# Performance work log

Hardware: AMD Instinct MI355X
Metric: run time of the kernel (lower is better)

Reference implementation:

```python
import jax, jax.numpy as jnp
import numpy as np

BN_EPS = 1e-5
CLAMP = 1e-10


def _three_nn(q, p):
    # q: (B,N,3) query points, p: (B,M,3) reference points
    # returns dist (B,N,3) euclidean distance to 3 nearest, idx (B,N,3)
    d2 = (jnp.sum(q * q, -1)[:, :, None] + jnp.sum(p * p, -1)[:, None, :]
          - 2.0 * jnp.einsum('bnd,bmd->bnm', q, p))  # (B,N,M)
    neg_vals, idx = jax.lax.top_k(-d2, 3)
    dist = jnp.sqrt(jnp.maximum(-neg_vals, 1e-20))
    return dist, idx


def _gather(feats_t, idx):
    # feats_t: (B,M,C), idx: (B,N,3) -> (B,N,3,C)
    return jax.vmap(lambda f, i: f[i])(feats_t, idx)


def _conv_bn_relu(x, W, b, g, beta):
    # x: (B,Cin,N); 1x1 Conv1d + BatchNorm1d (training-mode batch stats) + relu
    y = jnp.einsum('oc,bcn->bon', W, x) + b[None, :, None]
    mean = jnp.mean(y, axis=(0, 2), keepdims=True)
    var = jnp.mean((y - mean) ** 2, axis=(0, 2), keepdims=True)
    y = (y - mean) * jax.lax.rsqrt(var + BN_EPS)
    y = y * g[None, :, None] + beta[None, :, None]
    return jax.nn.relu(y)


def setup_inputs() -> dict:
    key = jax.random.key(0)
    ks = jax.random.split(key, 10)
    B, N, M, C2, C1 = 4, 8192, 2048, 256, 128
    inp = {
        'xyz1': jax.random.normal(ks[0], (B, 3, N), jnp.float32),
        'xyz2': jax.random.normal(ks[1], (B, 3, M), jnp.float32),
        'norm1': jax.random.normal(ks[2], (B, 3, N), jnp.float32),
        'norm2': jax.random.normal(ks[3], (B, 3, M), jnp.float32),
        'points1': jax.random.normal(ks[4], (B, C1, N), jnp.float32),
        'points2': jax.random.normal(ks[5], (B, C2, M), jnp.float32),
        'W0': jax.random.normal(ks[6], (256, C2 + C1), jnp.float32) * 0.05,
        'b0': jax.random.normal(ks[7], (256,), jnp.float32) * 0.05,
        'g0': jnp.ones((256,), jnp.float32),
        'be0': jnp.zeros((256,), jnp.float32),
        'W1': jax.random.normal(ks[8], (128, 256), jnp.float32) * 0.05,
        'b1': jax.random.normal(ks[9], (128,), jnp.float32) * 0.05,
        'g1': jnp.ones((128,), jnp.float32),
        'be1': jnp.zeros((128,), jnp.float32),
    }
    return inp


def reference(xyz1, xyz2, norm1, norm2, points1, points2,
              W0, b0, g0, be0, W1, b1, g1, be1):
    B, _, N = xyz1.shape
    # 3-NN search
    dist, idx = _three_nn(jnp.transpose(xyz1, (0, 2, 1)),
                          jnp.transpose(xyz2, (0, 2, 1)))  # (B,N,3)
    # normal distance between query normals and gathered neighbor normals
    grouped_norm = _gather(jnp.transpose(norm2, (0, 2, 1)), idx)        # (B,N,3,3)
    diff = jnp.transpose(norm1, (0, 2, 1))[:, :, None, :] - grouped_norm
    norm_dist = jnp.sqrt(jnp.sum(diff * diff, -1))                       # (B,N,3)
    # distance weights
    recip_dist = 1.0 / jnp.maximum(dist, CLAMP)
    weight = recip_dist / jnp.sum(recip_dist, 2, keepdims=True)
    # normal weights
    recip_nd = 1.0 / jnp.maximum(norm_dist, CLAMP)
    norm_weight = recip_nd / jnp.sum(recip_nd, 2, keepdims=True)
    weight = weight * norm_weight                                        # (B,N,3)
    # three_interpolate: weighted gather of points2
    gathered_pts = _gather(jnp.transpose(points2, (0, 2, 1)), idx)       # (B,N,3,C)
    interpolated = jnp.einsum('bnkc,bnk->bcn', gathered_pts, weight)     # (B,C,N)
    new_points = jnp.concatenate([interpolated, points1], axis=1)        # (B,C+C1,N)
    new_points = _conv_bn_relu(new_points, W0, b0, g0, be0)
    new_points = _conv_bn_relu(new_points, W1, b1, g1, be1)
    return new_points
```

## Files before the change

kernel.cpp:

```cpp
#include <hip/hip_runtime.h>
#include <hip/hip_bf16.h>
#include <cstdint>
#include <cstddef>

static constexpr int BB   = 4;
static constexpr int NN   = 8192;
static constexpr int MM   = 2048;
static constexpr int C1   = 128;
static constexpr int C2   = 256;
static constexpr int CH0  = C2 + C1;
static constexpr int O0   = 256;
static constexpr int O1   = 128;
static constexpr int NCOL = BB * NN;
static constexpr float BN_EPS = 1e-5f;

static constexpr int REC0 = 64;
static constexpr int REC1 = 32;

using u16 = unsigned short;
typedef __attribute__((ext_vector_type(8))) short short8;
typedef __attribute__((ext_vector_type(4))) float f32x4;

static __device__ __forceinline__ float bf2f(u16 u) {
    union { unsigned int i; float f; } v; v.i = ((unsigned int)u) << 16; return v.f;
}
static __device__ __forceinline__ u16 f2bf(float f) {
    union { float f; unsigned int i; } v; v.f = f;
    unsigned int r = (v.i + 0x7fffu + ((v.i >> 16) & 1u)) >> 16;
    return (u16)r;
}

__global__ __launch_bounds__(256) void fused_pre_kernel(
        const float* __restrict__ xyz1,  const float* __restrict__ xyz2,
        const float* __restrict__ norm1, const float* __restrict__ norm2,
        int* __restrict__ idxOut, float* __restrict__ wOut,
        const float* __restrict__ points2, u16* __restrict__ p2T,
        const float* __restrict__ points1, u16* __restrict__ p1T,
        const float* __restrict__ W0f, u16* __restrict__ W0b,
        const float* __restrict__ W1f, u16* __restrict__ W1b,
        float* __restrict__ part0, float* __restrict__ part1) {
#pragma clang fp contract(off)
    __shared__ union { float4 pts[1024]; float tile[32][33]; } sm;
    int id = blockIdx.x;
    int t  = threadIdx.x;

    if (id >= 7680) {
        int flat = (id - 7680) * 256 + t;
        if (flat < REC0 * 512) part0[flat] = 0.f;
        else part1[flat - REC0 * 512] = 0.f;
        return;
    }
    if (id >= 1024) {
        int pid = id - 1024;
        if (pid < 6144) {
            const float* in; u16* out; int R, C, b, c0, r0;
            if (pid < 2048) {
                in = points2; out = p2T; R = C2; C = MM;
                b = pid >> 9; int rem = pid & 511;
                c0 = (rem & 63) * 32; r0 = (rem >> 6) * 32;
            } else {
                int id2 = pid - 2048;
                in = points1; out = p1T; R = C1; C = NN;
                b = id2 >> 10; int rem = id2 & 1023;
                c0 = (rem & 255) * 32; r0 = (rem >> 8) * 32;
            }
            int tx = t & 31, ty = t >> 5;
            const float* pin = in + (size_t)b * R * C;
            u16* pout = out + (size_t)b * R * C;
#pragma unroll
            for (int j = 0; j < 4; ++j) {
                int r = ty + j * 8;
                sm.tile[r][tx] = pin[(size_t)(r0 + r) * C + (c0 + tx)];
            }
            __syncthreads();
#pragma unroll
            for (int j = 0; j < 4; ++j) {
                int c = ty + j * 8;
                pout[(size_t)(c0 + c) * R + (r0 + tx)] = f2bf(sm.tile[tx][c]);
            }
        } else {
            int i = (pid - 6144) * 256 + t;
            if (i < O0 * CH0) W0b[i] = f2bf(W0f[i]);
            else {
                int i2 = i - O0 * CH0;
                if (i2 < O1 * O0) W1b[i2] = f2bf(W1f[i2]);
            }
        }
        return;
    }

    int b    = id >> 8;
    int nblk = id & 255;
    int j    = t & 7;

    int n = nblk * 32 + (t >> 3);
    const float* x1 = xyz1 + (size_t)b * 3 * NN;
    float qx = x1[n], qy = x1[NN + n], qz = x1[2 * NN + n];
    float qq = __builtin_fmaf(qx, qx, __builtin_fmaf(qy, qy, qz * qz));

    const float* x2 = xyz2 + (size_t)b * 3 * MM;

    float d0 = 3.4e38f, d1 = 3.4e38f, d2v = 3.4e38f;
    int   i0 = 0, i1 = 0, i2 = 0;

    for (int chunk = 0; chunk < MM / 1024; ++chunk) {
        __syncthreads();
        for (int i = t; i < 1024; i += 256) {
            int m = chunk * 1024 + i;
            float px = x2[m];
            float py = x2[MM + m];
            float pz = x2[2 * MM + m];
            float pp = __builtin_fmaf(px, px, __builtin_fmaf(py, py, pz * pz));
            sm.pts[i] = make_float4(-2.0f * px, -2.0f * py, -2.0f * pz, pp);
        }
        __syncthreads();

#pragma unroll 8
        for (int s = 0; s < 1024 / 8; ++s) {
            int ml = s * 8 + j;
            float4 P = sm.pts[ml];
            float d  = __builtin_fmaf(qx, P.x,
                        __builtin_fmaf(qy, P.y,
                         __builtin_fmaf(qz, P.z, qq + P.w)));
            if (d < d2v) {
                int m = chunk * 1024 + ml;
                if (d < d1) {
                    if (d < d0) { d2v = d1; i2 = i1; d1 = d0; i1 = i0; d0 = d; i0 = m; }
                    else        { d2v = d1; i2 = i1; d1 = d;  i1 = m; }
                } else          { d2v = d;  i2 = m; }
            }
        }
    }

#pragma unroll
    for (int k = 1; k <= 4; k <<= 1) {
        float e0 = __shfl_xor(d0, k, 64), e1 = __shfl_xor(d1, k, 64), e2 = __shfl_xor(d2v, k, 64);
        int   f0 = __shfl_xor(i0, k, 64), f1 = __shfl_xor(i1, k, 64), f2 = __shfl_xor(i2, k, 64);
        float ed[3] = {e0, e1, e2}; int ef[3] = {f0, f1, f2};
#pragma unroll
        for (int e = 0; e < 3; ++e) {
            float dd = ed[e]; int ff = ef[e];
            bool b2 = (dd < d2v) || (dd == d2v && ff < i2);
            if (b2) {
                bool b1 = (dd < d1) || (dd == d1 && ff < i1);
                if (b1) {
                    d2v = d1; i2 = i1;
                    bool b0 = (dd < d0) || (dd == d0 && ff < i0);
                    if (b0) { d1 = d0; i1 = i0; d0 = dd; i0 = ff; }
                    else    { d1 = dd; i1 = ff; }
                } else { d2v = dd; i2 = ff; }
            }
        }
    }

    if (j == 0) {
        float s0 = sqrtf(fmaxf(d0, 1e-20f));
        float s1 = sqrtf(fmaxf(d1, 1e-20f));
        float s2 = sqrtf(fmaxf(d2v, 1e-20f));
        float r0 = 1.0f / fmaxf(s0, 1e-10f);
        float r1 = 1.0f / fmaxf(s1, 1e-10f);
        float r2 = 1.0f / fmaxf(s2, 1e-10f);
        float rs = (r0 + r1) + r2;
        float w0 = r0 / rs, w1 = r1 / rs, w2 = r2 / rs;

        const float* nm1 = norm1 + (size_t)b * 3 * NN;
        const float* nm2 = norm2 + (size_t)b * 3 * MM;
        float ax = nm1[n], ay = nm1[NN + n], az = nm1[2 * NN + n];
        float nd[3]; int ii[3] = {i0, i1, i2};
#pragma unroll
        for (int k = 0; k < 3; ++k) {
            int ik = ii[k];
            float dx = ax - nm2[ik];
            float dy = ay - nm2[MM + ik];
            float dz = az - nm2[2 * MM + ik];
            nd[k] = sqrtf((dx * dx + dy * dy) + dz * dz);
        }
        float m0 = 1.0f / fmaxf(nd[0], 1e-10f);
        float m1 = 1.0f / fmaxf(nd[1], 1e-10f);
        float m2 = 1.0f / fmaxf(nd[2], 1e-10f);
        float ms = (m0 + m1) + m2;

        int col = b * NN + n;
        idxOut[col * 3 + 0] = i0;
        idxOut[col * 3 + 1] = i1;
        idxOut[col * 3 + 2] = i2;
        wOut[col * 3 + 0] = w0 * (m0 / ms);
        wOut[col * 3 + 1] = w1 * (m1 / ms);
        wOut[col * 3 + 2] = w2 * (m2 / ms);
    }
}

__global__ __launch_bounds__(256, 2) void gemm0_kernel(
        const u16* __restrict__ A,
        const u16* __restrict__ Bt,
        const u16* __restrict__ p1T,
        const int* __restrict__ idx,
        const float* __restrict__ w,
        u16* __restrict__ Ct,
        const float* __restrict__ bias,
        float* __restrict__ partials) {
    constexpr int KDIM = CH0;
    constexpr int COLT = 64;
    constexpr int KT  = KDIM / 64;
    constexpr int NI  = COLT / 32;
    constexpr int ASZ = 256 * 64;
    constexpr int BSZ = COLT * 64;
    __shared__ u16 smem[2 * ASZ + 2 * BSZ];

    int t   = threadIdx.x;
    int l   = t & 63;
    int wv  = t >> 6;
    int rl  = l >> 3;
    int cg_ = ((l & 7) ^ rl) * 8;
    int cb0 = blockIdx.x * COLT;
    int lm  = l & 15;
    int q   = l >> 4;
    int wm0 = (wv & 1) * 64;
    int wn0 = (wv >> 1) * (COLT / 2);

    int colg = cb0 + (t >> 2);
    int vi0 = idx[colg * 3 + 0], vi1 = idx[colg * 3 + 1], vi2 = idx[colg * 3 + 2];
    float vw0 = w[colg * 3 + 0], vw1 = w[colg * 3 + 1], vw2 = w[colg * 3 + 2];
    const u16* p2base = Bt + (size_t)(cb0 >> 13) * MM * C2;

    auto stage = [&](int buf, int k0) {
#pragma unroll
        for (int iss = 0; iss < 8; ++iss) {
            int row = wv * 64 + iss * 8;
            const u16* g = A + (size_t)(row + rl) * KDIM + k0 + cg_;
            __builtin_amdgcn_global_load_lds(
                (const __attribute__((address_space(1))) unsigned int*)g,
                (__attribute__((address_space(3))) unsigned int*)(&smem[buf * ASZ + row * 64]),
                16, 0, 0);
        }
        if (k0 < C2) {
            int row = t >> 2;
            int kc  = (t & 3) * 16;
            const u16* bp = p2base + k0 + kc;
            const u16* r0p = bp + (size_t)vi0 * C2;
            const u16* r1p = bp + (size_t)vi1 * C2;
            const u16* r2p = bp + (size_t)vi2 * C2;
            union { uint4 v; u16 u[8]; } x0, x1, x2, y0, y1, y2, lo, hi;
            x0.v = *(const uint4*)r0p; y0.v = *(const uint4*)(r0p + 8);
            x1.v = *(const uint4*)r1p; y1.v = *(const uint4*)(r1p + 8);
            x2.v = *(const uint4*)r2p; y2.v = *(const uint4*)(r2p + 8);
#pragma unroll
            for (int e = 0; e < 8; ++e) {
                lo.u[e] = f2bf(vw0 * bf2f(x0.u[e]) + vw1 * bf2f(x1.u[e]) + vw2 * bf2f(x2.u[e]));
                hi.u[e] = f2bf(vw0 * bf2f(y0.u[e]) + vw1 * bf2f(y1.u[e]) + vw2 * bf2f(y2.u[e]));
            }
            int c0 = kc >> 3;
            u16* dstB = &smem[2 * ASZ + buf * BSZ + row * 64];
            *(uint4*)&dstB[((c0)     ^ (row & 7)) * 8] = lo.v;
            *(uint4*)&dstB[((c0 + 1) ^ (row & 7)) * 8] = hi.v;
        } else {
#pragma unroll
            for (int iss = 0; iss < 2; ++iss) {
                int row = wv * 16 + iss * 8;
                const u16* g = p1T + (size_t)(cb0 + row + rl) * C1 + (k0 - C2) + cg_;
                __builtin_amdgcn_global_load_lds(
                    (const __attribute__((address_space(1))) unsigned int*)g,
                    (__attribute__((address_space(3))) unsigned int*)(&smem[2 * ASZ + buf * BSZ + row * 64]),
                    16, 0, 0);
            }
        }
    };

    f32x4 acc[8][NI] = {};

    stage(0, 0);
    for (int kt = 0; kt < KT; ++kt) {
        __syncthreads();
        if (kt + 1 < KT) stage((kt + 1) & 1, (kt + 1) * 64);
        const u16* As = &smem[(kt & 1) * ASZ];
        const u16* Bs = &smem[2 * ASZ + (kt & 1) * BSZ];
#pragma unroll
        for (int ks = 0; ks < 2; ++ks) {
            int csw = ((ks * 4 + q) ^ (lm & 7)) * 8;
            short8 av[8], bv[NI];
#pragma unroll
            for (int mi = 0; mi < 8; ++mi) {
                int mrow = (mi >> 2) * 128 + wm0 + (mi & 3) * 16;
                av[mi] = *(const short8*)&As[(mrow + lm) * 64 + csw];
            }
#pragma unroll
            for (int ni = 0; ni < NI; ++ni)
                bv[ni] = *(const short8*)&Bs[(wn0 + ni * 16 + lm) * 64 + csw];
#pragma unroll
            for (int mi = 0; mi < 8; ++mi)
#pragma unroll
                for (int ni = 0; ni < NI; ++ni)
                    acc[mi][ni] = __builtin_amdgcn_mfma_f32_16x16x32_bf16(
                        av[mi], bv[ni], acc[mi][ni], 0, 0, 0);
        }
    }

    u16*   Cs   = smem;
    float* reds = (float*)&smem[COLT * 264];

    __syncthreads();
    reds[t] = 0.f; reds[256 + t] = 0.f;
    __syncthreads();

#pragma unroll
    for (int mi = 0; mi < 8; ++mi) {
        int chL = (mi >> 2) * 128 + wm0 + (mi & 3) * 16 + q * 4;
        float bv4[4];
#pragma unroll
        for (int r = 0; r < 4; ++r) bv4[r] = bias[chL + r];
        float s[4]  = {0.f, 0.f, 0.f, 0.f};
        float s2[4] = {0.f, 0.f, 0.f, 0.f};
#pragma unroll
        for (int ni = 0; ni < NI; ++ni) {
            int colL = wn0 + ni * 16 + lm;
            union { u16 u[4]; uint2 d; } pk;
#pragma unroll
            for (int r = 0; r < 4; ++r) {
                float v = acc[mi][ni][r] + bv4[r];
                s[r]  += v;
                s2[r] += v * v;
                pk.u[r] = f2bf(v);
            }
            *(uint2*)&Cs[colL * 264 + chL] = pk.d;
        }
#pragma unroll
        for (int r = 0; r < 4; ++r) {
            float a = s[r], b2 = s2[r];
#pragma unroll
            for (int off = 1; off < 16; off <<= 1) {
                a  += __shfl_xor(a, off, 64);
                b2 += __shfl_xor(b2, off, 64);
            }
            if (lm == 0) {
                atomicAdd(&reds[chL + r], a);
                atomicAdd(&reds[256 + chL + r], b2);
            }
        }
    }
    __syncthreads();

    {
        int c = t >> 2, h = t & 3;
        const u16* src = &Cs[c * 264 + h * 64];
        u16* dst = Ct + (size_t)(cb0 + c) * O0 + h * 64;
#pragma unroll
        for (int jj = 0; jj < 8; ++jj)
            *(uint4*)(dst + jj * 8) = *(const uint4*)(src + jj * 8);
    }
    int recIdx = blockIdx.x & (REC0 - 1);
    atomicAdd(&partials[(size_t)recIdx * 512 + t], reds[t]);
    atomicAdd(&partials[(size_t)recIdx * 512 + 256 + t], reds[256 + t]);
}

__global__ __launch_bounds__(256) void gemm1_kernel(const u16* __restrict__ A,
                                                    const u16* __restrict__ Bt,
                                                    u16* __restrict__ Ct,
                                                    const float* __restrict__ bias,
                                                    const float* __restrict__ redB,
                                                    const float* __restrict__ gB,
                                                    const float* __restrict__ beB,
                                                    float invN,
                                                    float* __restrict__ partials) {
    constexpr int KDIM = O0;
    constexpr int COLT = 64;
    constexpr int KT  = KDIM / 64;
    constexpr int NI  = COLT / 32;
    constexpr int ASZ = 128 * 64;
    constexpr int BSZ = COLT * 64;
    __shared__ u16 smem[2 * ASZ + 2 * BSZ];
    __shared__ float sSc[KDIM];
    __shared__ float sSh[KDIM];

    int t   = threadIdx.x;
    int l   = t & 63;
    int wv  = t >> 6;
    int rl  = l >> 3;
    int cg_ = ((l & 7) ^ rl) * 8;
    int cb0 = blockIdx.x * COLT;
    int lm  = l & 15;
    int q   = l >> 4;
    int wm0 = (wv & 1) * 64;
    int wn0 = (wv >> 1) * (COLT / 2);

    {
        float s = 0.f, s2 = 0.f;
#pragma unroll 8
        for (int i = 0; i < REC0; ++i) {
            s  += redB[i * 512 + t];
            s2 += redB[i * 512 + 256 + t];
        }
        float mean = s * invN;
        float var  = fmaxf(s2 * invN - mean * mean, 0.f);
        float inv  = rsqrtf(var + BN_EPS);
        float sc   = gB[t] * inv;
        sSc[t] = sc;
        sSh[t] = beB[t] - mean * sc;
        __syncthreads();
    }

    auto stage = [&](int buf, int k0) {
#pragma unroll
        for (int iss = 0; iss < 4; ++iss) {
            int row = wv * 32 + iss * 8;
            const u16* g = A + (size_t)(row + rl) * KDIM + k0 + cg_;
            __builtin_amdgcn_global_load_lds(
                (const __attribute__((address_space(1))) unsigned int*)g,
                (__attribute__((address_space(3))) unsigned int*)(&smem[buf * ASZ + row * 64]),
                16, 0, 0);
        }
        {
            int row = t >> 2;
            int kc  = (t & 3) * 16;
            const u16* gp = Bt + (size_t)(cb0 + row) * KDIM + k0 + kc;
            union { uint4 v; u16 u[8]; } lo, hi;
            lo.v = *(const uint4*)gp;
            hi.v = *(const uint4*)(gp + 8);
#pragma unroll
            for (int e = 0; e < 8; ++e) {
                float f0 = bf2f(lo.u[e]);
                lo.u[e] = f2bf(fmaxf(f0 * sSc[k0 + kc + e] + sSh[k0 + kc + e], 0.f));
                float f1 = bf2f(hi.u[e]);
                hi.u[e] = f2bf(fmaxf(f1 * sSc[k0 + kc + 8 + e] + sSh[k0 + kc + 8 + e], 0.f));
            }
            int c0 = kc >> 3;
            u16* dstB = &smem[2 * ASZ + buf * BSZ + row * 64];
            *(uint4*)&dstB[((c0)     ^ (row & 7)) * 8] = lo.v;
            *(uint4*)&dstB[((c0 + 1) ^ (row & 7)) * 8] = hi.v;
        }
    };

    f32x4 acc[4][NI] = {};

    stage(0, 0);
    for (int kt = 0; kt < KT; ++kt) {
        __syncthreads();
        if (kt + 1 < KT) stage((kt + 1) & 1, (kt + 1) * 64);
        const u16* As = &smem[(kt & 1) * ASZ];
        const u16* Bs = &smem[2 * ASZ + (kt & 1) * BSZ];
#pragma unroll
        for (int ks = 0; ks < 2; ++ks) {
            int csw = ((ks * 4 + q) ^ (lm & 7)) * 8;
            short8 av[4], bv[NI];
#pragma unroll
            for (int mi = 0; mi < 4; ++mi)
                av[mi] = *(const short8*)&As[(wm0 + mi * 16 + lm) * 64 + csw];
#pragma unroll
            for (int ni = 0; ni < NI; ++ni)
                bv[ni] = *(const short8*)&Bs[(wn0 + ni * 16 + lm) * 64 + csw];
#pragma unroll
            for (int mi = 0; mi < 4; ++mi)
#pragma unroll
                for (int ni = 0; ni < NI; ++ni)
                    acc[mi][ni] = __builtin_amdgcn_mfma_f32_16x16x32_bf16(
                        av[mi], bv[ni], acc[mi][ni], 0, 0, 0);
        }
    }

    u16*   Cs   = smem;
    float* reds = (float*)&smem[COLT * 136];

    __syncthreads();
    if (t < 256) reds[t] = 0.f;
    __syncthreads();

#pragma unroll
    for (int mi = 0; mi < 4; ++mi) {
        int chL = wm0 + mi * 16 + q * 4;
        float bv4[4];
#pragma unroll
        for (int r = 0; r < 4; ++r) bv4[r] = bias[chL + r];
        float s[4]  = {0.f, 0.f, 0.f, 0.f};
        float s2[4] = {0.f, 0.f, 0.f, 0.f};
#pragma unroll
        for (int ni = 0; ni < NI; ++ni) {
            int colL = wn0 + ni * 16 + lm;
            union { u16 u[4]; uint2 d; } pk;
#pragma unroll
            for (int r = 0; r < 4; ++r) {
                float v = acc[mi][ni][r] + bv4[r];
                s[r]  += v;
                s2[r] += v * v;
                pk.u[r] = f2bf(v);
            }
            *(uint2*)&Cs[colL * 136 + chL] = pk.d;
        }
#pragma unroll
        for (int r = 0; r < 4; ++r) {
            float a = s[r], b2 = s2[r];
#pragma unroll
            for (int off = 1; off < 16; off <<= 1) {
                a  += __shfl_xor(a, off, 64);
                b2 += __shfl_xor(b2, off, 64);
            }
            if (lm == 0) {
                atomicAdd(&reds[chL + r], a);
                atomicAdd(&reds[128 + chL + r], b2);
            }
        }
    }
    __syncthreads();

    for (int u = t; u < COLT * 2; u += 256) {
        int c = u >> 1, h = u & 1;
        const u16* src = &Cs[c * 136 + h * 64];
        u16* dst = Ct + (size_t)(cb0 + c) * O1 + h * 64;
#pragma unroll
        for (int jj = 0; jj < 8; ++jj)
            *(uint4*)(dst + jj * 8) = *(const uint4*)(src + jj * 8);
    }
    int recIdx = blockIdx.x & (REC1 - 1);
    atomicAdd(&partials[(size_t)recIdx * 256 + t], reds[t]);
}

__global__ __launch_bounds__(256) void finalize_kernel(const u16* __restrict__ y1T,
                                                       const float* __restrict__ part1,
                                                       const float* __restrict__ g1,
                                                       const float* __restrict__ be1,
                                                       float invN,
                                                       float* __restrict__ out) {
    __shared__ float tile[64][129];
    __shared__ float sc[O1], sh[O1];
    int t  = threadIdx.x;
    int b  = blockIdx.y;
    int n0 = blockIdx.x * 64;

    if (t < O1) {
        float s = 0.f, s2 = 0.f;
#pragma unroll 8
        for (int i = 0; i < REC1; ++i) {
            s  += part1[i * 256 + t];
            s2 += part1[i * 256 + 128 + t];
        }
        float mean = s * invN;
        float var  = fmaxf(s2 * invN - mean * mean, 0.f);
        float inv  = rsqrtf(var + BN_EPS);
        float scv  = g1[t] * inv;
        sc[t] = scv;
        sh[t] = be1[t] - mean * scv;
    }
    __syncthreads();

#pragma unroll
    for (int it = 0; it < 32; ++it) {
        int flat = it * 256 + t;
        int cl = flat >> 7;
        int c  = flat & 127;
        int col = b * NN + n0 + cl;
        float v = bf2f(y1T[(size_t)col * O1 + c]);
        tile[cl][c] = fmaxf(v * sc[c] + sh[c], 0.f);
    }
    __syncthreads();
#pragma unroll
    for (int it = 0; it < 32; ++it) {
        int flat = it * 256 + t;
        int c  = flat >> 6;
        int nl = flat & 63;
        out[(size_t)b * O1 * NN + (size_t)c * NN + n0 + nl] = tile[nl][c];
    }
}

extern "C" void kernel_launch(void* const* d_in, const int* in_sizes, int n_in,
                              void* d_out, int out_size, void* d_ws, size_t ws_size,
                              hipStream_t stream) {
    (void)in_sizes; (void)n_in; (void)out_size; (void)ws_size;

    const float* xyz1    = (const float*)d_in[0];
    const float* xyz2    = (const float*)d_in[1];
    const float* norm1   = (const float*)d_in[2];
    const float* norm2   = (const float*)d_in[3];
    const float* points1 = (const float*)d_in[4];
    const float* points2 = (const float*)d_in[5];
    const float* W0f     = (const float*)d_in[6];
    const float* b0      = (const float*)d_in[7];
    const float* g0      = (const float*)d_in[8];
    const float* be0     = (const float*)d_in[9];
    const float* W1f     = (const float*)d_in[10];
    const float* b1      = (const float*)d_in[11];
    const float* g1      = (const float*)d_in[12];
    const float* be1     = (const float*)d_in[13];
    float* out = (float*)d_out;

    char* w8 = (char*)d_ws;
    size_t off = 0;
    auto carve = [&](size_t bytes) { void* p = w8 + off; off += (bytes + 255) & ~(size_t)255; return p; };
    int*   idxW   = (int*)  carve((size_t)NCOL * 3 * sizeof(int));
    float* wW     = (float*)carve((size_t)NCOL * 3 * sizeof(float));
    u16*   p2T    = (u16*)  carve((size_t)BB * MM * C2 * 2);
    u16*   p1T    = (u16*)  carve((size_t)BB * NN * C1 * 2);
    u16*   W0b    = (u16*)  carve((size_t)O0 * CH0 * 2);
    u16*   W1b    = (u16*)  carve((size_t)O1 * O0 * 2);
    u16*   y0T    = (u16*)  carve((size_t)NCOL * O0 * 2);
    u16*   y1T    = (u16*)  carve((size_t)NCOL * O1 * 2);
    float* part0  = (float*)carve((size_t)REC0 * 512 * sizeof(float));
    float* part1  = (float*)carve((size_t)REC1 * 256 * sizeof(float));

    const float invN = 1.0f / (float)NCOL;

    fused_pre_kernel<<<7840, 256, 0, stream>>>(
        xyz1, xyz2, norm1, norm2, idxW, wW,
        points2, p2T, points1, p1T, W0f, W0b, W1f, W1b, part0, part1);

    gemm0_kernel<<<NCOL / 64, 256, 0, stream>>>(
        W0b, p2T, p1T, idxW, wW, y0T, b0, part0);

    gemm1_kernel<<<NCOL / 64, 256, 0, stream>>>(
        W1b, y0T, y1T, b1, part0, g0, be0, invN, part1);

    finalize_kernel<<<dim3(NN / 64, BB), 256, 0, stream>>>(y1T, part1, g1, be1, invN, out);
}
```

Measured before the change: 180.8 us.

## Split three-point interpolation out of GEMM0 into a separate kernel

```diff
diff --git a/kernel.cpp b/kernel.cpp
--- a/kernel.cpp
+++ b/kernel.cpp
@@ -190,12 +190,41 @@
     }
 }
 
+__global__ __launch_bounds__(256) void interp_kernel(
+        const u16* __restrict__ p2T,
+        const int* __restrict__ idx,
+        const float* __restrict__ w,
+        u16* __restrict__ xI) {
+    int t   = threadIdx.x;
+    int col = blockIdx.x * 32 + (t >> 3);
+    int kc  = (t & 7) * 32;
+
+    int vi0 = idx[col * 3 + 0], vi1 = idx[col * 3 + 1], vi2 = idx[col * 3 + 2];
+    float vw0 = w[col * 3 + 0], vw1 = w[col * 3 + 1], vw2 = w[col * 3 + 2];
+
+    const u16* bp  = p2T + (size_t)(col >> 13) * MM * C2 + kc;
+    const u16* r0p = bp + (size_t)vi0 * C2;
+    const u16* r1p = bp + (size_t)vi1 * C2;
+    const u16* r2p = bp + (size_t)vi2 * C2;
+    u16* dst = xI + (size_t)col * C2 + kc;
+
+#pragma unroll
+    for (int jj = 0; jj < 4; ++jj) {
+        union { uint4 v; u16 u[8]; } x0, x1, x2, o;
+        x0.v = *(const uint4*)(r0p + jj * 8);
+        x1.v = *(const uint4*)(r1p + jj * 8);
+        x2.v = *(const uint4*)(r2p + jj * 8);
+#pragma unroll
+        for (int e = 0; e < 8; ++e)
+            o.u[e] = f2bf(vw0 * bf2f(x0.u[e]) + vw1 * bf2f(x1.u[e]) + vw2 * bf2f(x2.u[e]));
+        *(uint4*)(dst + jj * 8) = o.v;
+    }
+}
+
 __global__ __launch_bounds__(256, 2) void gemm0_kernel(
         const u16* __restrict__ A,
-        const u16* __restrict__ Bt,
+        const u16* __restrict__ xI,
         const u16* __restrict__ p1T,
-        const int* __restrict__ idx,
-        const float* __restrict__ w,
         u16* __restrict__ Ct,
         const float* __restrict__ bias,
         float* __restrict__ partials) {
@@ -218,11 +247,6 @@
     int wm0 = (wv & 1) * 64;
     int wn0 = (wv >> 1) * (COLT / 2);
 
-    int colg = cb0 + (t >> 2);
-    int vi0 = idx[colg * 3 + 0], vi1 = idx[colg * 3 + 1], vi2 = idx[colg * 3 + 2];
-    float vw0 = w[colg * 3 + 0], vw1 = w[colg * 3 + 1], vw2 = w[colg * 3 + 2];
-    const u16* p2base = Bt + (size_t)(cb0 >> 13) * MM * C2;
-
     auto stage = [&](int buf, int k0) {
 #pragma unroll
         for (int iss = 0; iss < 8; ++iss) {
@@ -233,36 +257,16 @@
                 (__attribute__((address_space(3))) unsigned int*)(&smem[buf * ASZ + row * 64]),
                 16, 0, 0);
         }
-        if (k0 < C2) {
-            int row = t >> 2;
-            int kc  = (t & 3) * 16;
-            const u16* bp = p2base + k0 + kc;
-            const u16* r0p = bp + (size_t)vi0 * C2;
-            const u16* r1p = bp + (size_t)vi1 * C2;
-            const u16* r2p = bp + (size_t)vi2 * C2;
-            union { uint4 v; u16 u[8]; } x0, x1, x2, y0, y1, y2, lo, hi;
-            x0.v = *(const uint4*)r0p; y0.v = *(const uint4*)(r0p + 8);
-            x1.v = *(const uint4*)r1p; y1.v = *(const uint4*)(r1p + 8);
-            x2.v = *(const uint4*)r2p; y2.v = *(const uint4*)(r2p + 8);
-#pragma unroll
-            for (int e = 0; e < 8; ++e) {
-                lo.u[e] = f2bf(vw0 * bf2f(x0.u[e]) + vw1 * bf2f(x1.u[e]) + vw2 * bf2f(x2.u[e]));
-                hi.u[e] = f2bf(vw0 * bf2f(y0.u[e]) + vw1 * bf2f(y1.u[e]) + vw2 * bf2f(y2.u[e]));
-            }
-            int c0 = kc >> 3;
-            u16* dstB = &smem[2 * ASZ + buf * BSZ + row * 64];
-            *(uint4*)&dstB[((c0)     ^ (row & 7)) * 8] = lo.v;
-            *(uint4*)&dstB[((c0 + 1) ^ (row & 7)) * 8] = hi.v;
-        } else {
-#pragma unroll
-            for (int iss = 0; iss < 2; ++iss) {
-                int row = wv * 16 + iss * 8;
-                const u16* g = p1T + (size_t)(cb0 + row + rl) * C1 + (k0 - C2) + cg_;
-                __builtin_amdgcn_global_load_lds(
-                    (const __attribute__((address_space(1))) unsigned int*)g,
-                    (__attribute__((address_space(3))) unsigned int*)(&smem[2 * ASZ + buf * BSZ + row * 64]),
-                    16, 0, 0);
-            }
+#pragma unroll
+        for (int iss = 0; iss < 2; ++iss) {
+            int row = wv * 16 + iss * 8;
+            const u16* g = (k0 < C2)
+                ? xI  + (size_t)(cb0 + row + rl) * C2 + k0 + cg_
+                : p1T + (size_t)(cb0 + row + rl) * C1 + (k0 - C2) + cg_;
+            __builtin_amdgcn_global_load_lds(
+                (const __attribute__((address_space(1))) unsigned int*)g,
+                (__attribute__((address_space(3))) unsigned int*)(&smem[2 * ASZ + buf * BSZ + row * 64]),
+                16, 0, 0);
         }
     };
 
@@ -590,9 +594,10 @@
     u16*   W0b    = (u16*)  carve((size_t)O0 * CH0 * 2);
     u16*   W1b    = (u16*)  carve((size_t)O1 * O0 * 2);
     u16*   y0T    = (u16*)  carve((size_t)NCOL * O0 * 2);
-    u16*   y1T    = (u16*)  carve((size_t)NCOL * O1 * 2);
+    u16*   xI     = (u16*)  carve((size_t)NCOL * C2 * 2);
     float* part0  = (float*)carve((size_t)REC0 * 512 * sizeof(float));
     float* part1  = (float*)carve((size_t)REC1 * 256 * sizeof(float));
+    u16*   y1T    = xI;
 
     const float invN = 1.0f / (float)NCOL;
 
@@ -600,8 +605,10 @@
         xyz1, xyz2, norm1, norm2, idxW, wW,
         points2, p2T, points1, p1T, W0f, W0b, W1f, W1b, part0, part1);
 
+    interp_kernel<<<NCOL / 32, 256, 0, stream>>>(p2T, idxW, wW, xI);
+
     gemm0_kernel<<<NCOL / 64, 256, 0, stream>>>(
-        W0b, p2T, p1T, idxW, wW, y0T, b0, part0);
+        W0b, xI, p1T, y0T, b0, part0);
 
     gemm1_kernel<<<NCOL / 64, 256, 0, stream>>>(
         W1b, y0T, y1T, b1, part0, g0, be0, invN, part1);
```

New measurement: 189.3 us. 4.7% more time.
